# Performance work log

Hardware: AMD Instinct MI355X
Metric: run time of the kernel (lower is better)

## Reference

```python
import jax, jax.numpy as jnp
import numpy as np
from jax import lax

SZ, SENLEN, V, DWE, DPE, MAXPOS, DEE, DR, DC, KLOC = 2048, 128, 50000, 100, 5, 256, 100, 34, 300, 10
CIN = DWE + 2 * DPE + DEE  # 210


def setup_inputs() -> dict:
    key = jax.random.key(0)
    ks = jax.random.split(key, 16)
    inp = jax.random.randint(ks[0], (SZ, SENLEN), 0, V, dtype=jnp.int32)
    pos1 = jax.random.randint(ks[1], (SZ, SENLEN), 0, MAXPOS, dtype=jnp.int32)
    pos2 = jax.random.randint(ks[2], (SZ, SENLEN), 0, MAXPOS, dtype=jnp.int32)
    loc = jax.random.randint(ks[3], (SZ, KLOC), 0, V, dtype=jnp.int32)
    loc_mark = jax.random.randint(ks[4], (SZ,), 1, 6, dtype=jnp.int32)  # 1..5, keeps 4+mark < KLOC
    subtype = jax.random.randint(ks[5], (SZ,), 0, DR, dtype=jnp.int32)
    # piecewise L/M/R sentence masks around two cut points
    a = jax.random.randint(ks[6], (SZ, 1), 1, SENLEN // 2, dtype=jnp.int32)
    b = jax.random.randint(ks[7], (SZ, 1), SENLEN // 2, SENLEN - 1, dtype=jnp.int32)
    ar = jnp.arange(SENLEN)[None, :]
    maskL = (ar < a).astype(jnp.float32)
    maskM = ((ar >= a) & (ar < b)).astype(jnp.float32)
    maskR = (ar >= b).astype(jnp.float32)
    word_emb = 0.1 * jax.random.normal(ks[8], (V, DWE), dtype=jnp.float32)
    pos_emb = 0.1 * jax.random.normal(ks[9], (MAXPOS, DPE), dtype=jnp.float32)
    event_emb = 0.1 * jax.random.normal(ks[10], (DR, DEE), dtype=jnp.float32)
    conv_w = (1.0 / np.sqrt(CIN * 3)) * jax.random.normal(ks[11], (DC, CIN, 3), dtype=jnp.float32)
    conv_b = 0.01 * jax.random.normal(ks[12], (DC,), dtype=jnp.float32)
    return dict(inp=inp, pos1=pos1, pos2=pos2, loc=loc, loc_mark=loc_mark, subtype=subtype,
                maskL=maskL, maskM=maskM, maskR=maskR, word_emb=word_emb, pos_emb=pos_emb,
                event_emb=event_emb, conv_w=conv_w, conv_b=conv_b)


def reference(inp, pos1, pos2, loc, loc_mark, subtype, maskL, maskM, maskR,
              word_emb, pos_emb, event_emb, conv_w, conv_b):
    # padding_idx=0 semantics
    W = word_emb.at[0].set(0.0)
    E = event_emb.at[0].set(0.0)

    embeds = W[inp]                       # (SZ, L, DWE)
    p1 = pos_emb[pos1]                    # (SZ, L, DPE)
    p2 = pos_emb[pos2]                    # (SZ, L, DPE)

    # ragged loc feature: l[4] <- mean(l[4:4+mark]); l[5] <- l[4+mark]; keep l[0:6]
    loc_e = W[loc]                        # (SZ, K, DWE)
    j = jnp.arange(KLOC)[None, :]
    sel = ((j >= 4) & (j < 4 + loc_mark[:, None])).astype(loc_e.dtype)  # (SZ, K)
    mean4 = jnp.einsum('skd,sk->sd', loc_e, sel) / loc_mark[:, None].astype(loc_e.dtype)
    new5 = jnp.take_along_axis(loc_e, (4 + loc_mark)[:, None, None], axis=1)[:, 0, :]
    loc_embeds = jnp.concatenate([loc_e[:, :4].reshape(loc_e.shape[0], -1), mean4, new5], axis=1)  # (SZ, 6*DWE)

    ev = jnp.broadcast_to(E[subtype][:, None, :], (subtype.shape[0], SENLEN, DEE))
    x = jnp.concatenate([embeds, p1, p2, ev], axis=2).transpose(0, 2, 1)  # (SZ, CIN, L)

    conved = lax.conv_general_dilated(x, conv_w, window_strides=(1,), padding=((1, 1),),
                                      dimension_numbers=('NCH', 'OIH', 'NCH'))
    conved = conved + conv_b[None, :, None]  # (SZ, DC, L)

    # (mask*x + 1) -> maxpool over L -> -1  ==  max over L of mask*x (the +/-1 cancels exactly)
    pooledL = jnp.max(conved * maskL[:, None, :], axis=2)
    pooledM = jnp.max(conved * maskM[:, None, :], axis=2)
    pooledR = jnp.max(conved * maskR[:, None, :], axis=2)
    pooled = jnp.concatenate([pooledL, pooledM, pooledR], axis=1)  # (SZ, 3*DC)

    rep = jnp.tanh(jnp.concatenate([pooled, loc_embeds], axis=1))  # dropout in eval = identity
    return rep
```

## Files before the change

kernel.cpp:

```cpp
#include <hip/hip_runtime.h>
#include <hip/hip_bf16.h>

#define SZ    2048
#define SLEN  128
#define DWE   100
#define DPE   5
#define DEE   100
#define DC    300
#define CIN   210
#define KLOC  10
#define OUTW  1500

#define CINP  224
#define LCOLS 232
#define LROWS 130
#define CPAD  320

typedef short short8 __attribute__((ext_vector_type(8)));
typedef float f32x4 __attribute__((ext_vector_type(4)));

static __device__ __forceinline__ unsigned short f2b(float f) {
  return __builtin_bit_cast(unsigned short, __float2bfloat16(f));
}

__global__ void prep_wk(const float* __restrict__ conv_w, unsigned short* __restrict__ wk) {
  int idx = blockIdx.x * 256 + threadIdx.x;
  if (idx >= 3 * CPAD * CINP) return;
  int i  = idx % CINP;
  int c  = (idx / CINP) % CPAD;
  int kk = idx / (CINP * CPAD);
  float v = 0.f;
  if (c < DC && i < CIN) v = conv_w[(c * CIN + i) * 3 + kk];
  wk[idx] = f2b(v);
}

__global__ __launch_bounds__(256, 2) void dmcnn_main(
    const int* __restrict__ inp, const int* __restrict__ pos1, const int* __restrict__ pos2,
    const int* __restrict__ loc, const int* __restrict__ loc_mark, const int* __restrict__ subtype,
    const float* __restrict__ maskL, const float* __restrict__ maskM, const float* __restrict__ maskR,
    const float* __restrict__ word_emb, const float* __restrict__ pos_emb,
    const float* __restrict__ event_emb, const float* __restrict__ conv_b,
    const unsigned short* __restrict__ wk, float* __restrict__ out)
{
  __shared__ unsigned short XT[LROWS * LCOLS];
  __shared__ float evf[DEE];

  const int s   = blockIdx.x;
  const int tid = threadIdx.x;

  for (int i = tid; i < (LROWS * LCOLS) / 4; i += 256) ((uint2*)XT)[i] = make_uint2(0u, 0u);
  const int stv = subtype[s];
  if (tid < DEE) evf[tid] = (stv == 0) ? 0.f : event_emb[stv * DEE + tid];
  __syncthreads();

  {
    const int t = tid >> 1, half = tid & 1;
    unsigned short* row = &XT[(t + 1) * LCOLS];
    const int w = inp[s * SLEN + t];
    if (w != 0) {
      const float* wp = word_emb + (size_t)w * DWE + half * 50;
      #pragma unroll
      for (int j = 0; j < 25; ++j) {
        float2 v = ((const float2*)wp)[j];
        unsigned u = (unsigned)f2b(v.x) | ((unsigned)f2b(v.y) << 16);
        *(unsigned*)&row[half * 50 + j * 2] = u;
      }
    }
    const int p = (half == 0 ? pos1 : pos2)[s * SLEN + t];
    const float* pp = pos_emb + p * DPE;
    #pragma unroll
    for (int d = 0; d < DPE; ++d) row[DWE + half * DPE + d] = f2b(pp[d]);
    #pragma unroll
    for (int j = 0; j < 25; ++j) {
      float x = evf[half * 50 + j * 2], y = evf[half * 50 + j * 2 + 1];
      unsigned u = (unsigned)f2b(x) | ((unsigned)f2b(y) << 16);
      *(unsigned*)&row[110 + half * 50 + j * 2] = u;
    }
  }
  __syncthreads();

  const int wv   = tid >> 6;
  const int lane = tid & 63;
  const int r16  = lane & 15, q16 = lane >> 4;

  f32x4 acc[5][8];
  #pragma unroll
  for (int ci = 0; ci < 5; ++ci)
    #pragma unroll
    for (int tt = 0; tt < 8; ++tt) acc[ci][tt] = (f32x4){0.f, 0.f, 0.f, 0.f};

  const int crow0 = 80 * wv + r16;
  #pragma unroll
  for (int kk = 0; kk < 3; ++kk) {
    for (int kt = 0; kt < 7; ++kt) {
      const int k0 = kt * 32 + q16 * 8;
      short8 a[5];
      #pragma unroll
      for (int ci = 0; ci < 5; ++ci)
        a[ci] = *(const short8*)&wk[(size_t)(kk * CPAD + crow0 + 16 * ci) * CINP + k0];
      #pragma unroll
      for (int tt = 0; tt < 8; ++tt) {
        short8 b = *(const short8*)&XT[(16 * tt + kk + r16) * LCOLS + k0];
        #pragma unroll
        for (int ci = 0; ci < 5; ++ci)
          acc[ci][tt] = __builtin_amdgcn_mfma_f32_16x16x32_bf16(a[ci], b, acc[ci][tt], 0, 0, 0);
      }
    }
  }

  float mL[8], mM[8], mR[8];
  #pragma unroll
  for (int tt = 0; tt < 8; ++tt) {
    const int t = 16 * tt + r16;
    mL[tt] = maskL[s * SLEN + t];
    mM[tt] = maskM[s * SLEN + t];
    mR[tt] = maskR[s * SLEN + t];
  }
  float* orow = out + (size_t)s * OUTW;
  #pragma unroll
  for (int ci = 0; ci < 5; ++ci) {
    #pragma unroll
    for (int r = 0; r < 4; ++r) {
      const int c = 80 * wv + 16 * ci + 4 * q16 + r;
      const float bias = (c < DC) ? conv_b[c] : 0.f;
      float vL = -1e30f, vM = -1e30f, vR = -1e30f;
      #pragma unroll
      for (int tt = 0; tt < 8; ++tt) {
        const float v = acc[ci][tt][r] + bias;
        vL = fmaxf(vL, mL[tt] * v);
        vM = fmaxf(vM, mM[tt] * v);
        vR = fmaxf(vR, mR[tt] * v);
      }
      #pragma unroll
      for (int off = 1; off < 16; off <<= 1) {
        vL = fmaxf(vL, __shfl_xor(vL, off));
        vM = fmaxf(vM, __shfl_xor(vM, off));
        vR = fmaxf(vR, __shfl_xor(vR, off));
      }
      if (r16 == 0 && c < DC) {
        orow[c]          = tanhf(vL);
        orow[DC + c]     = tanhf(vM);
        orow[2 * DC + c] = tanhf(vR);
      }
    }
  }

  const int mark = loc_mark[s];
  for (int j = tid; j < 600; j += 256) {
    float v;
    if (j < 400) {
      const int k = j / 100, d = j % 100;
      const int idx = loc[s * KLOC + k];
      v = (idx == 0) ? 0.f : word_emb[(size_t)idx * DWE + d];
    } else if (j < 500) {
      const int d = j - 400;
      float sum = 0.f;
      for (int k = 4; k < 4 + mark; ++k) {
        const int idx = loc[s * KLOC + k];
        sum += (idx == 0) ? 0.f : word_emb[(size_t)idx * DWE + d];
      }
      v = sum / (float)mark;
    } else {
      const int d = j - 500;
      const int idx = loc[s * KLOC + 4 + mark];
      v = (idx == 0) ? 0.f : word_emb[(size_t)idx * DWE + d];
    }
    orow[900 + j] = tanhf(v);
  }
}

extern "C" void kernel_launch(void* const* d_in, const int* in_sizes, int n_in,
                              void* d_out, int out_size, void* d_ws, size_t ws_size,
                              hipStream_t stream) {
  const int*   inp       = (const int*)d_in[0];
  const int*   pos1      = (const int*)d_in[1];
  const int*   pos2      = (const int*)d_in[2];
  const int*   loc       = (const int*)d_in[3];
  const int*   loc_mark  = (const int*)d_in[4];
  const int*   subtype   = (const int*)d_in[5];
  const float* maskL     = (const float*)d_in[6];
  const float* maskM     = (const float*)d_in[7];
  const float* maskR     = (const float*)d_in[8];
  const float* word_emb  = (const float*)d_in[9];
  const float* pos_emb   = (const float*)d_in[10];
  const float* event_emb = (const float*)d_in[11];
  const float* conv_w    = (const float*)d_in[12];
  const float* conv_b    = (const float*)d_in[13];

  unsigned short* wk = (unsigned short*)d_ws;
  float* out = (float*)d_out;

  prep_wk<<<(3 * CPAD * CINP + 255) / 256, 256, 0, stream>>>(conv_w, wk);
  dmcnn_main<<<SZ, 256, 0, stream>>>(inp, pos1, pos2, loc, loc_mark, subtype,
      maskL, maskM, maskR, word_emb, pos_emb, event_emb, conv_b, wk, out);
}
```

Baseline: 240.7 us.

## Precompute per-subtype event-embedding conv contribution and shrink conv K dimension

The event embedding is the same at every position of a sentence, so its convolution contribution (plus bias) is precomputed once per subtype by a new prep kernel. It is then added in the epilogue, with boundary corrections at the first and last positions for zero padding. This cuts the MFMA reduction from 224 to 128 channels and shrinks the shared-memory tile. Masks are replaced by cut points found with ballot/popcount, which relies on the masks being contiguous L/M/R segments. The pooling is also restructured so the cross-lane reduction runs over the row groups.

```diff
diff --git a/kernel.cpp b/kernel.cpp
--- a/kernel.cpp
+++ b/kernel.cpp
@@ -10,9 +10,10 @@
 #define CIN   210
 #define KLOC  10
 #define OUTW  1500
-
-#define CINP  224
-#define LCOLS 232
+#define DR    34
+
+#define KP    128
+#define LCOLS 136
 #define LROWS 130
 #define CPAD  320
 
@@ -25,13 +26,30 @@
 
 __global__ void prep_wk(const float* __restrict__ conv_w, unsigned short* __restrict__ wk) {
   int idx = blockIdx.x * 256 + threadIdx.x;
-  if (idx >= 3 * CPAD * CINP) return;
-  int i  = idx % CINP;
-  int c  = (idx / CINP) % CPAD;
-  int kk = idx / (CINP * CPAD);
+  if (idx >= 3 * CPAD * KP) return;
+  int i  = idx & (KP - 1);
+  int c  = (idx / KP) % CPAD;
+  int kk = idx / (KP * CPAD);
   float v = 0.f;
-  if (c < DC && i < CIN) v = conv_w[(c * CIN + i) * 3 + kk];
+  if (c < DC && i < 110) v = conv_w[(c * CIN + i) * 3 + kk];
   wk[idx] = f2b(v);
+}
+
+__global__ void prep_ev(const float* __restrict__ conv_w, const float* __restrict__ event_emb,
+                        const float* __restrict__ conv_b, float* __restrict__ evconv) {
+  int idx = blockIdx.x * 256 + threadIdx.x;
+  if (idx >= DR * 3 * DC) return;
+  int c  = idx % DC;
+  int kk = (idx / DC) % 3;
+  int st = idx / (3 * DC);
+  float v = 0.f;
+  if (st != 0) {
+    const float* wrow = conv_w + (c * CIN + 110) * 3 + kk;
+    const float* e = event_emb + st * DEE;
+    for (int i = 0; i < DEE; ++i) v += wrow[3 * i] * e[i];
+  }
+  if (kk == 1) v += conv_b[c];
+  evconv[idx] = v;
 }
 
 __global__ __launch_bounds__(256, 2) void dmcnn_main(
@@ -39,43 +57,49 @@
     const int* __restrict__ loc, const int* __restrict__ loc_mark, const int* __restrict__ subtype,
     const float* __restrict__ maskL, const float* __restrict__ maskM, const float* __restrict__ maskR,
     const float* __restrict__ word_emb, const float* __restrict__ pos_emb,
-    const float* __restrict__ event_emb, const float* __restrict__ conv_b,
-    const unsigned short* __restrict__ wk, float* __restrict__ out)
+    const unsigned short* __restrict__ wk, const float* __restrict__ evconv,
+    float* __restrict__ out)
 {
   __shared__ unsigned short XT[LROWS * LCOLS];
-  __shared__ float evf[DEE];
+  __shared__ int cw[4];
 
   const int s   = blockIdx.x;
   const int tid = threadIdx.x;
 
-  for (int i = tid; i < (LROWS * LCOLS) / 4; i += 256) ((uint2*)XT)[i] = make_uint2(0u, 0u);
-  const int stv = subtype[s];
-  if (tid < DEE) evf[tid] = (stv == 0) ? 0.f : event_emb[stv * DEE + tid];
-  __syncthreads();
+  if (tid < 64)        ((unsigned*)XT)[tid] = 0u;
+  else if (tid < 128)  ((unsigned*)(XT + 129 * LCOLS))[tid - 64] = 0u;
+
+  if (tid < 128) {
+    const int inL = maskL[s * SLEN + tid] > 0.5f;
+    const int inM = maskM[s * SLEN + tid] > 0.5f;
+    unsigned long long bL = __ballot(inL);
+    unsigned long long bM = __ballot(inM);
+    if ((tid & 63) == 0) {
+      cw[tid >> 6]     = __popcll(bL);
+      cw[2 + (tid >> 6)] = __popcll(bM);
+    }
+  }
 
   {
     const int t = tid >> 1, half = tid & 1;
     unsigned short* row = &XT[(t + 1) * LCOLS];
     const int w = inp[s * SLEN + t];
-    if (w != 0) {
-      const float* wp = word_emb + (size_t)w * DWE + half * 50;
-      #pragma unroll
-      for (int j = 0; j < 25; ++j) {
+    const float* wp = word_emb + (size_t)w * DWE + half * 50;
+    #pragma unroll
+    for (int j = 0; j < 25; ++j) {
+      unsigned u = 0u;
+      if (w != 0) {
         float2 v = ((const float2*)wp)[j];
-        unsigned u = (unsigned)f2b(v.x) | ((unsigned)f2b(v.y) << 16);
-        *(unsigned*)&row[half * 50 + j * 2] = u;
-      }
+        u = (unsigned)f2b(v.x) | ((unsigned)f2b(v.y) << 16);
+      }
+      *(unsigned*)&row[half * 50 + j * 2] = u;
     }
     const int p = (half == 0 ? pos1 : pos2)[s * SLEN + t];
     const float* pp = pos_emb + p * DPE;
     #pragma unroll
     for (int d = 0; d < DPE; ++d) row[DWE + half * DPE + d] = f2b(pp[d]);
     #pragma unroll
-    for (int j = 0; j < 25; ++j) {
-      float x = evf[half * 50 + j * 2], y = evf[half * 50 + j * 2 + 1];
-      unsigned u = (unsigned)f2b(x) | ((unsigned)f2b(y) << 16);
-      *(unsigned*)&row[110 + half * 50 + j * 2] = u;
-    }
+    for (int d = 0; d < 9; ++d) row[110 + 9 * half + d] = 0;
   }
   __syncthreads();
 
@@ -83,64 +107,65 @@
   const int lane = tid & 63;
   const int r16  = lane & 15, q16 = lane >> 4;
 
-  f32x4 acc[5][8];
+  f32x4 acc[8][5];
   #pragma unroll
-  for (int ci = 0; ci < 5; ++ci)
-    #pragma unroll
-    for (int tt = 0; tt < 8; ++tt) acc[ci][tt] = (f32x4){0.f, 0.f, 0.f, 0.f};
-
-  const int crow0 = 80 * wv + r16;
+  for (int tt = 0; tt < 8; ++tt)
+    #pragma unroll
+    for (int ci = 0; ci < 5; ++ci) acc[tt][ci] = (f32x4){0.f, 0.f, 0.f, 0.f};
+
+  const unsigned short* wbase = wk + (size_t)(80 * wv + r16) * KP + q16 * 8;
   #pragma unroll
-  for (int kk = 0; kk < 3; ++kk) {
-    for (int kt = 0; kt < 7; ++kt) {
-      const int k0 = kt * 32 + q16 * 8;
-      short8 a[5];
+  for (int ks = 0; ks < 12; ++ks) {
+    const int kk = ks >> 2, kt = ks & 3;
+    short8 wf[5];
+    #pragma unroll
+    for (int ci = 0; ci < 5; ++ci)
+      wf[ci] = *(const short8*)(wbase + (size_t)(kk * CPAD + 16 * ci) * KP + kt * 32);
+    #pragma unroll
+    for (int tt = 0; tt < 8; ++tt) {
+      short8 xf = *(const short8*)&XT[(16 * tt + r16 + kk) * LCOLS + kt * 32 + q16 * 8];
       #pragma unroll
       for (int ci = 0; ci < 5; ++ci)
-        a[ci] = *(const short8*)&wk[(size_t)(kk * CPAD + crow0 + 16 * ci) * CINP + k0];
+        acc[tt][ci] = __builtin_amdgcn_mfma_f32_16x16x32_bf16(xf, wf[ci], acc[tt][ci], 0, 0, 0);
+    }
+  }
+
+  const int acut = cw[0] + cw[1];
+  const int bcut = acut + cw[2] + cw[3];
+  const int st   = subtype[s];
+  const float* evc = evconv + (size_t)st * 3 * DC;
+  float* orow = out + (size_t)s * OUTW;
+
+  #pragma unroll
+  for (int ci = 0; ci < 5; ++ci) {
+    const int c = 80 * wv + 16 * ci + r16;
+    if (c < DC) {
+      const float s0 = evc[c], s1 = evc[DC + c], s2 = evc[2 * DC + c];
+      const float base = s0 + s1 + s2;
+      float rL = 0.f, rM = 0.f, rR = 0.f;
       #pragma unroll
       for (int tt = 0; tt < 8; ++tt) {
-        short8 b = *(const short8*)&XT[(16 * tt + kk + r16) * LCOLS + k0];
         #pragma unroll
-        for (int ci = 0; ci < 5; ++ci)
-          acc[ci][tt] = __builtin_amdgcn_mfma_f32_16x16x32_bf16(a[ci], b, acc[ci][tt], 0, 0, 0);
-      }
-    }
-  }
-
-  float mL[8], mM[8], mR[8];
-  #pragma unroll
-  for (int tt = 0; tt < 8; ++tt) {
-    const int t = 16 * tt + r16;
-    mL[tt] = maskL[s * SLEN + t];
-    mM[tt] = maskM[s * SLEN + t];
-    mR[tt] = maskR[s * SLEN + t];
-  }
-  float* orow = out + (size_t)s * OUTW;
-  #pragma unroll
-  for (int ci = 0; ci < 5; ++ci) {
-    #pragma unroll
-    for (int r = 0; r < 4; ++r) {
-      const int c = 80 * wv + 16 * ci + 4 * q16 + r;
-      const float bias = (c < DC) ? conv_b[c] : 0.f;
-      float vL = -1e30f, vM = -1e30f, vR = -1e30f;
+        for (int j = 0; j < 4; ++j) {
+          const int t = 16 * tt + 4 * q16 + j;
+          float v = acc[tt][ci][j] + base;
+          if (t == 0)   v -= s0;
+          if (t == 127) v -= s2;
+          if (t < acut)      rL = fmaxf(rL, v);
+          else if (t < bcut) rM = fmaxf(rM, v);
+          else               rR = fmaxf(rR, v);
+        }
+      }
       #pragma unroll
-      for (int tt = 0; tt < 8; ++tt) {
-        const float v = acc[ci][tt][r] + bias;
-        vL = fmaxf(vL, mL[tt] * v);
-        vM = fmaxf(vM, mM[tt] * v);
-        vR = fmaxf(vR, mR[tt] * v);
-      }
-      #pragma unroll
-      for (int off = 1; off < 16; off <<= 1) {
-        vL = fmaxf(vL, __shfl_xor(vL, off));
-        vM = fmaxf(vM, __shfl_xor(vM, off));
-        vR = fmaxf(vR, __shfl_xor(vR, off));
-      }
-      if (r16 == 0 && c < DC) {
-        orow[c]          = tanhf(vL);
-        orow[DC + c]     = tanhf(vM);
-        orow[2 * DC + c] = tanhf(vR);
+      for (int off = 16; off < 64; off <<= 1) {
+        rL = fmaxf(rL, __shfl_xor(rL, off));
+        rM = fmaxf(rM, __shfl_xor(rM, off));
+        rR = fmaxf(rR, __shfl_xor(rR, off));
+      }
+      if (q16 == 0) {
+        orow[c]          = tanhf(rL);
+        orow[DC + c]     = tanhf(rM);
+        orow[2 * DC + c] = tanhf(rR);
       }
     }
   }
@@ -188,9 +213,11 @@
   const float* conv_b    = (const float*)d_in[13];
 
   unsigned short* wk = (unsigned short*)d_ws;
+  float* evconv = (float*)((char*)d_ws + 3 * CPAD * KP * 2);
   float* out = (float*)d_out;
 
-  prep_wk<<<(3 * CPAD * CINP + 255) / 256, 256, 0, stream>>>(conv_w, wk);
+  prep_wk<<<(3 * CPAD * KP + 255) / 256, 256, 0, stream>>>(conv_w, wk);
+  prep_ev<<<(DR * 3 * DC + 255) / 256, 256, 0, stream>>>(conv_w, event_emb, conv_b, evconv);
   dmcnn_main<<<SZ, 256, 0, stream>>>(inp, pos1, pos2, loc, loc_mark, subtype,
-      maskL, maskM, maskR, word_emb, pos_emb, event_emb, conv_b, wk, out);
-}
+      maskL, maskM, maskR, word_emb, pos_emb, wk, evconv, out);
+}
```

Result: slower. 261.4 us (+8.6%).
